# Kernel tuning notes

Hardware: AMD Instinct MI355X
Metric: run time of the kernel (lower is better)

The kernel has to match this reference:

```python
import jax, jax.numpy as jnp
import numpy as np

B, S, HID, NH = 2, 2048, 1024, 16
HD = HID // NH
BASE = 10000.0


def _rope_tables(seq_len, head_dim):
    i = jnp.arange(0, head_dim, 2, dtype=jnp.float32)
    theta = BASE ** (-i / head_dim)
    pos = jnp.arange(seq_len, dtype=jnp.float32)
    m_theta = jnp.outer(pos, theta)  # [S, HD/2]
    cos = jnp.repeat(jnp.cos(m_theta), 2, axis=1)  # [S, HD]
    sin = jnp.repeat(jnp.sin(m_theta), 2, axis=1)
    return cos, sin


def _apply_rope(x, cos, sin):
    # x: [B, NH, S, HD]; interleaved rotation: (-x1, x0, -x3, x2, ...)
    x_even = x[..., 0::2]
    x_odd = x[..., 1::2]
    inv_x = jnp.stack((-x_odd, x_even), axis=-1).reshape(x.shape)
    return x * cos[None, None] + inv_x * sin[None, None]


def setup_inputs() -> dict:
    key = jax.random.key(0)
    ks = jax.random.split(key, 7)
    q = jax.random.normal(ks[0], (B, S, HID), dtype=jnp.float32)
    k = jax.random.normal(ks[1], (B, S, HID), dtype=jnp.float32)
    v = jax.random.normal(ks[2], (B, S, HID), dtype=jnp.float32)
    scale = 1.0 / np.sqrt(HID)
    Wq = jax.random.normal(ks[3], (HID, HID), dtype=jnp.float32) * scale
    Wk = jax.random.normal(ks[4], (HID, HID), dtype=jnp.float32) * scale
    Wv = jax.random.normal(ks[5], (HID, HID), dtype=jnp.float32) * scale
    Wo = jax.random.normal(ks[6], (HID, HID), dtype=jnp.float32) * scale
    mask = jnp.triu(jnp.ones((S, S), dtype=bool), k=1)[None, None]  # causal, True = masked
    return {"q": q, "k": k, "v": v, "mask": mask,
            "Wq": Wq, "Wk": Wk, "Wv": Wv, "Wo": Wo}


def reference(q, k, v, mask, Wq, Wk, Wv, Wo):
    cos, sin = _rope_tables(S, HD)
    # Linear (torch stores weight as [out, in]; y = x @ W.T)
    qh = (q @ Wq.T).reshape(B, S, NH, HD).transpose(0, 2, 1, 3)
    kh = (k @ Wk.T).reshape(B, S, NH, HD).transpose(0, 2, 1, 3)
    vh = (v @ Wv.T).reshape(B, S, NH, HD).transpose(0, 2, 1, 3)
    qh = _apply_rope(qh, cos, sin)
    kh = _apply_rope(kh, cos, sin)
    scores = jnp.einsum("bhqd,bhkd->bhqk", qh, kh) / np.sqrt(HD)
    neg_min = jnp.finfo(jnp.float32).min
    scores = jnp.where(mask, neg_min, scores)
    attn = jax.nn.softmax(scores, axis=-1)
    out = jnp.einsum("bhqk,bhkd->bhqd", attn, vh)  # [B,NH,S,HD]
    out = out.transpose(0, 2, 1, 3).reshape(B, S, HID)
    return out @ Wo.T
```

## Files before the change

kernel.cpp:

```cpp
#include <hip/hip_runtime.h>

#define S_LEN 2048
#define HIDN  1024
#define NHEAD 16
#define HDIM  64
#define MROWS 4096
#define KDIM  1024
#define NDIM  1024

typedef __attribute__((ext_vector_type(8))) short bf16x8;
typedef __attribute__((ext_vector_type(4))) float f32x4;

static __device__ __forceinline__ ushort f2bf(float f) {
    unsigned int u = __float_as_uint(f);
    u = (u + 0x7fffu + ((u >> 16) & 1u)) >> 16;
    return (ushort)u;
}
static __device__ __forceinline__ float bf2f(ushort u) {
    return __uint_as_float(((unsigned int)u) << 16);
}

static __device__ __forceinline__ void gload16(const ushort* g, ushort* l) {
    __builtin_amdgcn_global_load_lds(
        (const __attribute__((address_space(1))) unsigned int*)g,
        (__attribute__((address_space(3))) unsigned int*)l, 16, 0, 0);
}

__global__ __launch_bounds__(256) void prep_kernel(
    const float* __restrict__ q, const float* __restrict__ k,
    const float* __restrict__ v, const float* __restrict__ Wq,
    const float* __restrict__ Wk, const float* __restrict__ Wv,
    const float* __restrict__ Wo,
    ushort* __restrict__ qb, ushort* __restrict__ kb, ushort* __restrict__ vb,
    ushort* __restrict__ Wqb, ushort* __restrict__ Wkb, ushort* __restrict__ Wvb,
    ushort* __restrict__ Wob,
    float* __restrict__ rc, float* __restrict__ rs)
{
    const long Q4 = (long)MROWS * KDIM / 4;
    const long W4 = (long)NDIM * KDIM / 4;
    if (blockIdx.x < 16384) {
        long i = (long)blockIdx.x * 256 + threadIdx.x;
        const float* src; ushort* dst; long off;
        if (i < Q4)          { src = q; dst = qb; off = i; }
        else if (i < 2 * Q4) { src = k; dst = kb; off = i - Q4; }
        else if (i < 3 * Q4) { src = v; dst = vb; off = i - 2 * Q4; }
        else {
            long t = i - 3 * Q4;
            int wsel = (int)(t >> 18);
            off = t & (W4 - 1);
            src = (wsel == 0) ? Wq : (wsel == 1) ? Wk : (wsel == 2) ? Wv : Wo;
            dst = (wsel == 0) ? Wqb : (wsel == 1) ? Wkb : (wsel == 2) ? Wvb : Wob;
        }
        float4 vv = ((const float4*)src)[off];
        ushort4 o;
        o.x = f2bf(vv.x); o.y = f2bf(vv.y); o.z = f2bf(vv.z); o.w = f2bf(vv.w);
        ((ushort4*)dst)[off] = o;
    } else {
        int idx = (blockIdx.x - 16384) * 256 + threadIdx.x;
        int s  = idx >> 5;
        int jp = idx & 31;
        float theta = expf(-(float)(2 * jp) * (9.210340371976184f / 64.0f));
        float ang = (float)s * theta;
        float sv, cv;
        sincosf(ang, &sv, &cv);
        rc[idx] = cv;
        rs[idx] = sv;
    }
}

static __device__ __forceinline__ void gemm_mainloop(
    const ushort* __restrict__ A, const ushort* __restrict__ W,
    ushort* As, ushort* Bs, f32x4 (&acc)[2][4],
    int m0, int n0, int tid)
{
    const int lane = tid & 63, wid = tid >> 6;
    const int wm = wid & 1, wn = wid >> 1;
    const int quad = lane >> 4, l15 = lane & 15;

    for (int k0 = 0; k0 < KDIM; k0 += 64) {
        __syncthreads();
#pragma unroll
        for (int rr = 0; rr < 2; ++rr) {
            int sidx = tid + rr * 256;
            int row = sidx >> 3;
            int g = (sidx & 7) ^ (row & 7);
            gload16(A + (size_t)(m0 + row) * KDIM + k0 + g * 8, As + sidx * 8);
        }
#pragma unroll
        for (int rr = 0; rr < 4; ++rr) {
            int sidx = tid + rr * 256;
            int row = sidx >> 3;
            int g = (sidx & 7) ^ (row & 7);
            gload16(W + (size_t)(n0 + row) * KDIM + k0 + g * 8, Bs + sidx * 8);
        }
        __syncthreads();

#pragma unroll
        for (int ks = 0; ks < 2; ++ks) {
            bf16x8 af[2], bfr[4];
#pragma unroll
            for (int i = 0; i < 2; ++i) {
                int row = wm * 32 + i * 16 + l15;
                int gg = ((ks << 2) | quad) ^ (row & 7);
                af[i] = *(const bf16x8*)&As[row * 64 + gg * 8];
            }
#pragma unroll
            for (int j = 0; j < 4; ++j) {
                int row = wn * 64 + j * 16 + l15;
                int gg = ((ks << 2) | quad) ^ (row & 7);
                bfr[j] = *(const bf16x8*)&Bs[row * 64 + gg * 8];
            }
#pragma unroll
            for (int i = 0; i < 2; ++i)
#pragma unroll
                for (int j = 0; j < 4; ++j)
                    acc[i][j] = __builtin_amdgcn_mfma_f32_16x16x32_bf16(
                        af[i], bfr[j], acc[i][j], 0, 0, 0);
        }
    }
}

__global__ __launch_bounds__(256) void gemm_qkv(
    const ushort* __restrict__ qb, const ushort* __restrict__ kb,
    const ushort* __restrict__ vb,
    const ushort* __restrict__ Wqb, const ushort* __restrict__ Wkb,
    const ushort* __restrict__ Wvb,
    ushort* __restrict__ Qh, ushort* __restrict__ Kh, ushort* __restrict__ Vt,
    const float* __restrict__ rc, const float* __restrict__ rs)
{
    __shared__ __align__(16) ushort As[64 * 64];
    __shared__ __align__(16) ushort Bs[128 * 64];

    const int tid = threadIdx.x;
    const int lane = tid & 63, wid = tid >> 6;
    const int wm = wid & 1, wn = wid >> 1;
    const int quad = lane >> 4, l15 = lane & 15;
    const int z = blockIdx.z;

    const ushort* A; const ushort* W; int m0, n0;
    if (z == 2) {
        m0 = ((int)blockIdx.y * 2 + ((int)blockIdx.x >> 5)) * 64;
        n0 = ((int)blockIdx.x & 31) * 128;
        A = Wvb; W = vb;
    } else {
        m0 = blockIdx.x * 64; n0 = blockIdx.y * 128;
        A = (z == 0) ? qb : kb;
        W = (z == 0) ? Wqb : Wkb;
    }

    f32x4 acc[2][4];
#pragma unroll
    for (int i = 0; i < 2; ++i)
#pragma unroll
        for (int j = 0; j < 4; ++j) acc[i][j] = 0.0f;

    gemm_mainloop(A, W, As, Bs, acc, m0, n0, tid);

    if (z != 2) {
        ushort* out = (z == 0) ? Qh : Kh;
        const float scale = (z == 0) ? 0.18033688011112042f : 1.0f;
#pragma unroll
        for (int i = 0; i < 2; ++i)
#pragma unroll
            for (int j = 0; j < 4; ++j)
#pragma unroll
                for (int r = 0; r < 4; ++r) {
                    int m = m0 + wm * 32 + i * 16 + quad * 4 + r;
                    int n = n0 + wn * 64 + j * 16 + l15;
                    float v = acc[i][j][r];
                    int b = m >> 11, s = m & (S_LEN - 1);
                    int h = n >> 6, d = n & 63;
                    int pidx = s * 32 + (d >> 1);
                    float cv = rc[pidx], sv = rs[pidx];
                    float partner = __shfl_xor(v, 1);
                    v = (d & 1) ? (v * cv + partner * sv)
                                : (v * cv - partner * sv);
                    out[((size_t)((b * NHEAD + h) * S_LEN + s)) * HDIM + d] =
                        f2bf(v * scale);
                }
    } else {
#pragma unroll
        for (int i = 0; i < 2; ++i)
#pragma unroll
            for (int j = 0; j < 4; ++j)
#pragma unroll
                for (int r = 0; r < 4; ++r) {
                    int m = m0 + wm * 32 + i * 16 + quad * 4 + r;
                    int n = n0 + wn * 64 + j * 16 + l15;
                    int h = m >> 6, d = m & 63;
                    int b = n >> 11, s = n & (S_LEN - 1);
                    Vt[((size_t)((b * NHEAD + h) * HDIM + d)) * S_LEN + s] =
                        f2bf(acc[i][j][r]);
                }
    }
}

__global__ __launch_bounds__(256) void gemm_out(
    const ushort* __restrict__ A, const ushort* __restrict__ W,
    float* __restrict__ out)
{
    __shared__ __align__(16) ushort As[64 * 64];
    __shared__ __align__(16) ushort Bs[128 * 64];

    const int tid = threadIdx.x;
    const int lane = tid & 63, wid = tid >> 6;
    const int wm = wid & 1, wn = wid >> 1;
    const int quad = lane >> 4, l15 = lane & 15;
    const int m0 = blockIdx.x * 64, n0 = blockIdx.y * 128;

    f32x4 acc[2][4];
#pragma unroll
    for (int i = 0; i < 2; ++i)
#pragma unroll
        for (int j = 0; j < 4; ++j) acc[i][j] = 0.0f;

    gemm_mainloop(A, W, As, Bs, acc, m0, n0, tid);

#pragma unroll
    for (int i = 0; i < 2; ++i)
#pragma unroll
        for (int j = 0; j < 4; ++j)
#pragma unroll
            for (int r = 0; r < 4; ++r) {
                int m = m0 + wm * 32 + i * 16 + quad * 4 + r;
                int n = n0 + wn * 64 + j * 16 + l15;
                out[(size_t)m * NDIM + n] = acc[i][j][r];
            }
}

__global__ __launch_bounds__(256) void attn_mfma(
    const ushort* __restrict__ Qh, const ushort* __restrict__ Kh,
    const ushort* __restrict__ Vt,
    ushort* __restrict__ O0, ushort* __restrict__ O1,
    float* __restrict__ L0, float* __restrict__ L1)
{
    __shared__ __align__(16) ushort Ks[64 * 64];
    __shared__ __align__(16) ushort Vs[64 * 64];
    __shared__ __align__(16) ushort Ps[64 * 72];

    const int tid = threadIdx.x;
    const int lane = tid & 63, w = tid >> 6;
    const int quad = lane >> 4, l15 = lane & 15;
    const int id = blockIdx.x;
    const int h = id & 15, b = (id >> 4) & 1, t = id >> 5;

    int seg, y;
    if (t < 32) { seg = (t & 1) ? 0 : 1; y = (t & 1) ? 31 - (t >> 1) : (t >> 1); }
    else { int u = t - 32; seg = (u & 1) ? 0 : 1;
           y = (u & 1) ? 15 - (u >> 1) : 16 + (u >> 1); }

    const int qt = seg ? (31 - y) : y;
    const int lo = seg ? ((33 - y) >> 1) : 0;
    const int hi = seg ? (32 - y) : ((y + 2) >> 1);
    const int q0 = qt * 64;
    const size_t hoff = (size_t)(b * NHEAD + h) * S_LEN * HDIM;

    bf16x8 ones;
#pragma unroll
    for (int i = 0; i < 8; ++i) ones[i] = (short)0x3F80;

    bf16x8 qf[2];
#pragma unroll
    for (int ks = 0; ks < 2; ++ks)
        qf[ks] = *(const bf16x8*)(Qh + hoff +
            (size_t)(q0 + w * 16 + l15) * HDIM + ks * 32 + quad * 8);

    f32x4 Oa[4];
    f32x4 Lacc = 0.0f;
#pragma unroll
    for (int j = 0; j < 4; ++j) Oa[j] = 0.0f;

    const int rowq = q0 + w * 16 + quad * 4;

    for (int kt = lo; kt < hi; ++kt) {
        const int k0 = kt * 64;
        const bool diag = (kt == qt);
        __syncthreads();
#pragma unroll
        for (int rr = 0; rr < 2; ++rr) {
            int sidx = tid + rr * 256;
            int row = sidx >> 3;
            int g = (sidx & 7) ^ (row & 7);
            gload16(Kh + hoff + (size_t)(k0 + row) * HDIM + g * 8, Ks + sidx * 8);
            gload16(Vt + hoff + (size_t)row * S_LEN + k0 + g * 8, Vs + sidx * 8);
        }
        __syncthreads();

        f32x4 Sa[4];
#pragma unroll
        for (int j = 0; j < 4; ++j) Sa[j] = 0.0f;
#pragma unroll
        for (int ks = 0; ks < 2; ++ks) {
            const int p = ((ks << 2) | quad) ^ (l15 & 7);
            bf16x8 kf[4];
#pragma unroll
            for (int j = 0; j < 4; ++j)
                kf[j] = *(const bf16x8*)&Ks[(j * 16 + l15) * 64 + p * 8];
#pragma unroll
            for (int j = 0; j < 4; ++j)
                Sa[j] = __builtin_amdgcn_mfma_f32_16x16x32_bf16(qf[ks], kf[j],
                                                                Sa[j], 0, 0, 0);
        }

#pragma unroll
        for (int j = 0; j < 4; ++j) {
#pragma unroll
            for (int r = 0; r < 4; ++r) {
                float p = exp2f(Sa[j][r]);
                if (diag) {
                    int key = k0 + j * 16 + l15;
                    if (key > rowq + r) p = 0.f;
                }
                Ps[(w * 16 + quad * 4 + r) * 72 + j * 16 + l15] =
                    (ushort)(__float_as_uint(p) >> 16);
            }
        }

#pragma unroll
        for (int ks = 0; ks < 2; ++ks) {
            const int p = ((ks << 2) | quad) ^ (l15 & 7);
            bf16x8 pf = *(const bf16x8*)&Ps[(w * 16 + l15) * 72 + ks * 32 + quad * 8];
            bf16x8 vf[4];
#pragma unroll
            for (int j = 0; j < 4; ++j)
                vf[j] = *(const bf16x8*)&Vs[(j * 16 + l15) * 64 + p * 8];
#pragma unroll
            for (int j = 0; j < 4; ++j)
                Oa[j] = __builtin_amdgcn_mfma_f32_16x16x32_bf16(pf, vf[j],
                                                                Oa[j], 0, 0, 0);
            Lacc = __builtin_amdgcn_mfma_f32_16x16x32_bf16(pf, ones, Lacc, 0, 0, 0);
        }
    }

    ushort* Op = seg ? O1 : O0;
    float*  Lp = seg ? L1 : L0;
    const size_t rbase = ((size_t)(b * NHEAD + h) * S_LEN + rowq);
#pragma unroll
    for (int r = 0; r < 4; ++r) {
#pragma unroll
        for (int j = 0; j < 4; ++j)
            Op[(rbase + r) * HDIM + j * 16 + l15] = f2bf(Oa[j][r]);
        if (l15 == 0) Lp[rbase + r] = Lacc[r];
    }
}

__global__ __launch_bounds__(256) void combine_kernel(
    const ushort* __restrict__ O0, const ushort* __restrict__ O1,
    const float* __restrict__ L0, const float* __restrict__ L1,
    ushort* __restrict__ AO)
{
    int flat = blockIdx.x * 256 + threadIdx.x;
    int row = flat >> 4;
    int dq = (flat & 15) * 4;
    int bh = row >> 11, s = row & (S_LEN - 1);
    int b = bh >> 4, h = bh & 15;
    ushort4 a = *(const ushort4*)(O0 + (size_t)row * HDIM + dq);
    ushort4 c = *(const ushort4*)(O1 + (size_t)row * HDIM + dq);
    float inv = 1.0f / (L0[row] + L1[row]);
    ushort4 o;
    o.x = f2bf((bf2f(a.x) + bf2f(c.x)) * inv);
    o.y = f2bf((bf2f(a.y) + bf2f(c.y)) * inv);
    o.z = f2bf((bf2f(a.z) + bf2f(c.z)) * inv);
    o.w = f2bf((bf2f(a.w) + bf2f(c.w)) * inv);
    *(ushort4*)(AO + ((size_t)(b * S_LEN + s)) * HIDN + h * HDIM + dq) = o;
}

extern "C" void kernel_launch(void* const* d_in, const int* in_sizes, int n_in,
                              void* d_out, int out_size, void* d_ws, size_t ws_size,
                              hipStream_t stream) {
    const float* qf  = (const float*)d_in[0];
    const float* kf  = (const float*)d_in[1];
    const float* vf  = (const float*)d_in[2];
    const float* Wqf = (const float*)d_in[4];
    const float* Wkf = (const float*)d_in[5];
    const float* Wvf = (const float*)d_in[6];
    const float* Wof = (const float*)d_in[7];
    float* out = (float*)d_out;

    char* wsp = (char*)d_ws;
    float* rc = (float*)wsp;            wsp += 65536 * 4;
    float* rs = (float*)wsp;            wsp += 65536 * 4;
    ushort* qb  = (ushort*)wsp;         wsp += (size_t)MROWS * KDIM * 2;
    ushort* kb  = (ushort*)wsp;         wsp += (size_t)MROWS * KDIM * 2;
    ushort* vb  = (ushort*)wsp;         wsp += (size_t)MROWS * KDIM * 2;
    ushort* Wqb = (ushort*)wsp;         wsp += (size_t)NDIM * KDIM * 2;
    ushort* Wkb = (ushort*)wsp;         wsp += (size_t)NDIM * KDIM * 2;
    ushort* Wvb = (ushort*)wsp;         wsp += (size_t)NDIM * KDIM * 2;
    ushort* Wob = (ushort*)wsp;         wsp += (size_t)NDIM * KDIM * 2;
    ushort* Qh  = (ushort*)wsp;         wsp += (size_t)MROWS * HIDN * 2;
    ushort* Kh  = (ushort*)wsp;         wsp += (size_t)MROWS * HIDN * 2;
    ushort* Vt  = (ushort*)wsp;         wsp += (size_t)MROWS * HIDN * 2;
    ushort* AO  = (ushort*)wsp;

    ushort* O0 = qb;
    ushort* O1 = kb;
    float*  L0 = (float*)vb;
    float*  L1 = (float*)vb + 65536;

    prep_kernel<<<16640, 256, 0, stream>>>(qf, kf, vf, Wqf, Wkf, Wvf, Wof,
                                           qb, kb, vb, Wqb, Wkb, Wvb, Wob, rc, rs);

    gemm_qkv<<<dim3(64, 8, 3), 256, 0, stream>>>(
        qb, kb, vb, Wqb, Wkb, Wvb, Qh, Kh, Vt, rc, rs);

    attn_mfma<<<2048, 256, 0, stream>>>(Qh, Kh, Vt, O0, O1, L0, L1);

    combine_kernel<<<4096, 256, 0, stream>>>(O0, O1, L0, L1, AO);

    gemm_out<<<dim3(64, 8), 256, 0, stream>>>(AO, Wob, out);
}
```

Measured before the change: 219.5 us.

## Fuse split-KV combine into output projection GEMM and trim attention address math

Removes the separate combine kernel and folds the two-segment merge (sum of partial outputs scaled by the reciprocal of summed denominators) into the A-tile load of the output GEMM, which writes the merged bf16 values into shared memory itself. This drops one kernel launch and a round trip of the intermediate attention output through global memory. The A tile now goes through registers instead of async global-to-LDS loads, and the 8 N-blocks each redo the merge for the same rows. The attention kernel also hoists the K/V pointer arithmetic out of the loop, uses the hardware exp2 intrinsic, and precomputes the P-tile LDS pointers.

New measurement: 213.3 us. 1.03x faster.

```diff
diff --git a/kernel.cpp b/kernel.cpp
--- a/kernel.cpp
+++ b/kernel.cpp
@@ -196,8 +196,9 @@
 }
 
 __global__ __launch_bounds__(256) void gemm_out(
-    const ushort* __restrict__ A, const ushort* __restrict__ W,
-    float* __restrict__ out)
+    const ushort* __restrict__ O0, const ushort* __restrict__ O1,
+    const float* __restrict__ L0, const float* __restrict__ L1,
+    const ushort* __restrict__ W, float* __restrict__ out)
 {
     __shared__ __align__(16) ushort As[64 * 64];
     __shared__ __align__(16) ushort Bs[128 * 64];
@@ -214,7 +215,65 @@
 #pragma unroll
         for (int j = 0; j < 4; ++j) acc[i][j] = 0.0f;
 
-    gemm_mainloop(A, W, As, Bs, acc, m0, n0, tid);
+    for (int k0 = 0; k0 < KDIM; k0 += 64) {
+        const int h = k0 >> 6;
+        bf16x8 a0[2], a1[2];
+        float li[2];
+#pragma unroll
+        for (int rr = 0; rr < 2; ++rr) {
+            int sidx = tid + rr * 256;
+            int row = sidx >> 3;
+            int g = (sidx & 7) ^ (row & 7);
+            int m = m0 + row, bb = m >> 11, s = m & (S_LEN - 1);
+            size_t rowO = (size_t)(bb * NHEAD + h) * S_LEN + s;
+            a0[rr] = *(const bf16x8*)(O0 + rowO * HDIM + g * 8);
+            a1[rr] = *(const bf16x8*)(O1 + rowO * HDIM + g * 8);
+            li[rr] = __builtin_amdgcn_rcpf(L0[rowO] + L1[rowO]);
+        }
+        __syncthreads();
+#pragma unroll
+        for (int rr = 0; rr < 2; ++rr) {
+            int sidx = tid + rr * 256;
+            bf16x8 packed;
+#pragma unroll
+            for (int e = 0; e < 8; ++e) {
+                float f = (bf2f((ushort)a0[rr][e]) + bf2f((ushort)a1[rr][e])) * li[rr];
+                packed[e] = (short)(__float_as_uint(f) >> 16);
+            }
+            *(bf16x8*)&As[sidx * 8] = packed;
+        }
+#pragma unroll
+        for (int rr = 0; rr < 4; ++rr) {
+            int sidx = tid + rr * 256;
+            int row = sidx >> 3;
+            int g = (sidx & 7) ^ (row & 7);
+            gload16(W + (size_t)(n0 + row) * KDIM + k0 + g * 8, Bs + sidx * 8);
+        }
+        __syncthreads();
+
+#pragma unroll
+        for (int ks = 0; ks < 2; ++ks) {
+            bf16x8 af[2], bfr[4];
+#pragma unroll
+            for (int i = 0; i < 2; ++i) {
+                int row = wm * 32 + i * 16 + l15;
+                int gg = ((ks << 2) | quad) ^ (row & 7);
+                af[i] = *(const bf16x8*)&As[row * 64 + gg * 8];
+            }
+#pragma unroll
+            for (int j = 0; j < 4; ++j) {
+                int row = wn * 64 + j * 16 + l15;
+                int gg = ((ks << 2) | quad) ^ (row & 7);
+                bfr[j] = *(const bf16x8*)&Bs[row * 64 + gg * 8];
+            }
+#pragma unroll
+            for (int i = 0; i < 2; ++i)
+#pragma unroll
+                for (int j = 0; j < 4; ++j)
+                    acc[i][j] = __builtin_amdgcn_mfma_f32_16x16x32_bf16(
+                        af[i], bfr[j], acc[i][j], 0, 0, 0);
+        }
+    }
 
 #pragma unroll
     for (int i = 0; i < 2; ++i)
@@ -272,6 +331,18 @@
 
     const int rowq = q0 + w * 16 + quad * 4;
 
+    const ushort* kg[2]; const ushort* vg[2];
+#pragma unroll
+    for (int rr = 0; rr < 2; ++rr) {
+        int sidx = tid + rr * 256;
+        int row = sidx >> 3;
+        int gsw = (sidx & 7) ^ (row & 7);
+        kg[rr] = Kh + hoff + (size_t)(lo * 64 + row) * HDIM + gsw * 8;
+        vg[rr] = Vt + hoff + (size_t)row * S_LEN + lo * 64 + gsw * 8;
+    }
+    ushort* psw = Ps + (w * 16 + quad * 4) * 72;
+    const ushort* psr = Ps + (w * 16 + l15) * 72;
+
     for (int kt = lo; kt < hi; ++kt) {
         const int k0 = kt * 64;
         const bool diag = (kt == qt);
@@ -279,10 +350,10 @@
 #pragma unroll
         for (int rr = 0; rr < 2; ++rr) {
             int sidx = tid + rr * 256;
-            int row = sidx >> 3;
-            int g = (sidx & 7) ^ (row & 7);
-            gload16(Kh + hoff + (size_t)(k0 + row) * HDIM + g * 8, Ks + sidx * 8);
-            gload16(Vt + hoff + (size_t)row * S_LEN + k0 + g * 8, Vs + sidx * 8);
+            gload16(kg[rr], Ks + sidx * 8);
+            gload16(vg[rr], Vs + sidx * 8);
+            kg[rr] += 64 * HDIM;
+            vg[rr] += 64;
         }
         __syncthreads();
 
@@ -306,20 +377,19 @@
         for (int j = 0; j < 4; ++j) {
 #pragma unroll
             for (int r = 0; r < 4; ++r) {
-                float p = exp2f(Sa[j][r]);
+                float p = __builtin_amdgcn_exp2f(Sa[j][r]);
                 if (diag) {
                     int key = k0 + j * 16 + l15;
                     if (key > rowq + r) p = 0.f;
                 }
-                Ps[(w * 16 + quad * 4 + r) * 72 + j * 16 + l15] =
-                    (ushort)(__float_as_uint(p) >> 16);
+                psw[r * 72 + j * 16 + l15] = (ushort)(__float_as_uint(p) >> 16);
             }
         }
 
 #pragma unroll
         for (int ks = 0; ks < 2; ++ks) {
             const int p = ((ks << 2) | quad) ^ (l15 & 7);
-            bf16x8 pf = *(const bf16x8*)&Ps[(w * 16 + l15) * 72 + ks * 32 + quad * 8];
+            bf16x8 pf = *(const bf16x8*)&psr[ks * 32 + quad * 8];
             bf16x8 vf[4];
 #pragma unroll
             for (int j = 0; j < 4; ++j)
@@ -342,27 +412,6 @@
             Op[(rbase + r) * HDIM + j * 16 + l15] = f2bf(Oa[j][r]);
         if (l15 == 0) Lp[rbase + r] = Lacc[r];
     }
-}
-
-__global__ __launch_bounds__(256) void combine_kernel(
-    const ushort* __restrict__ O0, const ushort* __restrict__ O1,
-    const float* __restrict__ L0, const float* __restrict__ L1,
-    ushort* __restrict__ AO)
-{
-    int flat = blockIdx.x * 256 + threadIdx.x;
-    int row = flat >> 4;
-    int dq = (flat & 15) * 4;
-    int bh = row >> 11, s = row & (S_LEN - 1);
-    int b = bh >> 4, h = bh & 15;
-    ushort4 a = *(const ushort4*)(O0 + (size_t)row * HDIM + dq);
-    ushort4 c = *(const ushort4*)(O1 + (size_t)row * HDIM + dq);
-    float inv = 1.0f / (L0[row] + L1[row]);
-    ushort4 o;
-    o.x = f2bf((bf2f(a.x) + bf2f(c.x)) * inv);
-    o.y = f2bf((bf2f(a.y) + bf2f(c.y)) * inv);
-    o.z = f2bf((bf2f(a.z) + bf2f(c.z)) * inv);
-    o.w = f2bf((bf2f(a.w) + bf2f(c.w)) * inv);
-    *(ushort4*)(AO + ((size_t)(b * S_LEN + s)) * HIDN + h * HDIM + dq) = o;
 }
 
 extern "C" void kernel_launch(void* const* d_in, const int* in_sizes, int n_in,
@@ -389,8 +438,7 @@
     ushort* Wob = (ushort*)wsp;         wsp += (size_t)NDIM * KDIM * 2;
     ushort* Qh  = (ushort*)wsp;         wsp += (size_t)MROWS * HIDN * 2;
     ushort* Kh  = (ushort*)wsp;         wsp += (size_t)MROWS * HIDN * 2;
-    ushort* Vt  = (ushort*)wsp;         wsp += (size_t)MROWS * HIDN * 2;
-    ushort* AO  = (ushort*)wsp;
+    ushort* Vt  = (ushort*)wsp;
 
     ushort* O0 = qb;
     ushort* O1 = kb;
@@ -405,7 +453,5 @@
 
     attn_mfma<<<2048, 256, 0, stream>>>(Qh, Kh, Vt, O0, O1, L0, L1);
 
-    combine_kernel<<<4096, 256, 0, stream>>>(O0, O1, L0, L1, AO);
-
-    gemm_out<<<dim3(64, 8), 256, 0, stream>>>(AO, Wob, out);
-}
+    gemm_out<<<dim3(64, 8), 256, 0, stream>>>(O0, O1, L0, L1, Wob, out);
+}
```
